# Kernel tuning notes

Hardware: AMD Instinct MI355X
Metric: run time of the kernel (lower is better)

Reference implementation:

```python
import jax, jax.numpy as jnp
import numpy as np

NNZ = 819200
NUM_SESS = 16384
ITEMS_NUM = 1000000
EMB_DIM = 64


def setup_inputs() -> dict:
    key = jax.random.key(0)
    k1, k2, k3, k4 = jax.random.split(key, 4)
    row_idx = jnp.sort(jax.random.randint(k1, (NNZ,), 0, NUM_SESS, dtype=jnp.int32))
    col_idx = jax.random.randint(k2, (NNZ,), 0, ITEMS_NUM, dtype=jnp.int32)
    data_tensor = jax.random.uniform(k3, (NNZ,), dtype=jnp.float32)
    embeddings = jax.random.normal(k4, (ITEMS_NUM, EMB_DIM), dtype=jnp.float32)
    return {
        "row_idx": row_idx,
        "col_idx": col_idx,
        "data_tensor": data_tensor,
        "num_ids": NUM_SESS,
        "embeddings": embeddings,
    }


def reference(row_idx, col_idx, data_tensor, num_ids, embeddings):
    # sparse_coo([num_ids, ITEMS_NUM]) @ embeddings
    # == per-session weighted sum of gathered item embeddings.
    gathered = embeddings[col_idx]                      # [nnz, d]
    weighted = gathered * data_tensor[:, None]          # [nnz, d]
    user_embeddings = jax.ops.segment_sum(
        weighted, row_idx, num_segments=num_ids)        # [num_ids, d]
    return user_embeddings
```

## Files before the change

### kernel.cpp

```cpp
#include <hip/hip_runtime.h>


__global__ __launch_bounds__(256) void build_rowptr_kernel(
    const int* __restrict__ row_idx,
    int*       __restrict__ row_ptr,
    int nnz, int num_sess)
{
    int j = blockIdx.x * blockDim.x + threadIdx.x;
    if (j >= nnz) return;
    int r = row_idx[j];
    if (j == 0) {
        for (int s = 0; s <= r; ++s) row_ptr[s] = 0;
    } else {
        int rp = row_idx[j - 1];
        for (int s = rp + 1; s <= r; ++s) row_ptr[s] = j;
    }
    if (j == nnz - 1) {
        for (int s = r + 1; s <= num_sess; ++s) row_ptr[s] = nnz;
    }
}

__global__ __launch_bounds__(256, 8) void wsum_sess_kernel(
    const int*   __restrict__ row_ptr,
    const int*   __restrict__ col_idx,
    const float* __restrict__ data,
    const float* __restrict__ emb,
    float*       __restrict__ out,
    int num_sess)
{
    const int wave = threadIdx.x >> 6;
    const int lane = threadIdx.x & 63;
    const int sess = (blockIdx.x << 2) + wave;
    if (sess >= num_sess) return;

    const int start = row_ptr[sess];
    const int end   = row_ptr[sess + 1];

    float acc = 0.0f;

    for (int j0 = start; j0 < end; j0 += 64) {
        const int jl    = j0 + lane;
        const bool valid = (jl < end);
        int   col = valid ? col_idx[jl] : 0;
        float w   = valid ? data[jl]    : 0.0f;
        const int rem = end - j0;

        #pragma unroll
        for (int kb = 0; kb < 64; kb += 32) {
            if (kb >= rem) break;
            float v[32];
            float wk[32];
            #pragma unroll
            for (int k = 0; k < 32; ++k) {
                int c = __builtin_amdgcn_readlane(col, kb + k);
                wk[k] = __int_as_float(
                            __builtin_amdgcn_readlane(__float_as_int(w), kb + k));
                v[k] = emb[(size_t)c * 64 + lane];
            }
            #pragma unroll
            for (int k = 0; k < 32; ++k)
                acc += wk[k] * v[k];
        }
    }

    out[(size_t)sess * 64 + lane] = acc;
}

extern "C" void kernel_launch(void* const* d_in, const int* in_sizes, int n_in,
                              void* d_out, int out_size, void* d_ws, size_t ws_size,
                              hipStream_t stream) {
    const int*   row_idx = (const int*)  d_in[0];
    const int*   col_idx = (const int*)  d_in[1];
    const float* data    = (const float*)d_in[2];
    const float* emb     = (const float*)d_in[4];

    const int nnz      = in_sizes[0];
    const int num_sess = out_size / 64;

    int* row_ptr = (int*)d_ws;

    build_rowptr_kernel<<<(nnz + 255) / 256, 256, 0, stream>>>(
        row_idx, row_ptr, nnz, num_sess);

    const int blocks = (num_sess + 3) / 4;
    wsum_sess_kernel<<<blocks, 256, 0, stream>>>(
        row_ptr, col_idx, data, emb, (float*)d_out, num_sess);
}
```

Measured before the change: 335.7 us.

## Bucket nonzeros by embedding row and stream the table through shared memory

Replaces the random per-nonzero embedding gather with a bucket sort of nonzeros by column block. A histogram, a scan and a scatter group the nonzeros by bucket. A materialize kernel then loads each 128-row window of the embedding table into shared memory and writes the weighted rows to a per-nonzero scratch buffer, and a final kernel segment-sums that buffer per session. The aim is to turn scattered row reads into sequential streaming of the table. The cost is reading the entire table, a large scratch write and re-read, extra atomics and several more launches, and it needs a much larger workspace.

Result: slower. 546.2 us (+62.7%).

```diff
diff --git a/kernel.cpp b/kernel.cpp
--- a/kernel.cpp
+++ b/kernel.cpp
@@ -1,12 +1,18 @@
 #include <hip/hip_runtime.h>
+#include <stdint.h>
 
 
-__global__ __launch_bounds__(256) void build_rowptr_kernel(
+#define RPB      128
+#define LOG_RPB  7
+
+__global__ __launch_bounds__(256) void k1_rowptr_hist(
     const int* __restrict__ row_idx,
-    int*       __restrict__ row_ptr,
+    const int* __restrict__ col_idx,
+    int* __restrict__ row_ptr,
+    int* __restrict__ hist,
     int nnz, int num_sess)
 {
-    int j = blockIdx.x * blockDim.x + threadIdx.x;
+    int j = blockIdx.x * 256 + threadIdx.x;
     if (j >= nnz) return;
     int r = row_idx[j];
     if (j == 0) {
@@ -18,52 +24,130 @@
     if (j == nnz - 1) {
         for (int s = r + 1; s <= num_sess; ++s) row_ptr[s] = nnz;
     }
+    atomicAdd(&hist[col_idx[j] >> LOG_RPB], 1);
 }
 
-__global__ __launch_bounds__(256, 8) void wsum_sess_kernel(
-    const int*   __restrict__ row_ptr,
+__global__ __launch_bounds__(1024) void k2_scan(
+    const int* __restrict__ hist,
+    int* __restrict__ bstart,
+    int* __restrict__ cursor,
+    int nb)
+{
+    __shared__ int tsum[1024];
+    int t = threadIdx.x;
+    int loc[8];
+    int base = t * 8;
+    int s = 0;
+    #pragma unroll
+    for (int k = 0; k < 8; ++k) {
+        int b = base + k;
+        int v = (b < nb) ? hist[b] : 0;
+        loc[k] = s;
+        s += v;
+    }
+    tsum[t] = s;
+    __syncthreads();
+    for (int off = 1; off < 1024; off <<= 1) {
+        int v = (t >= off) ? tsum[t - off] : 0;
+        __syncthreads();
+        tsum[t] += v;
+        __syncthreads();
+    }
+    int tbase = (t == 0) ? 0 : tsum[t - 1];
+    #pragma unroll
+    for (int k = 0; k < 8; ++k) {
+        int b = base + k;
+        if (b < nb) {
+            int st = tbase + loc[k];
+            bstart[b] = st;
+            cursor[b] = st;
+        }
+    }
+    if (t == 1023) bstart[nb] = tsum[1023];
+}
+
+__global__ __launch_bounds__(256) void k3_scatter(
     const int*   __restrict__ col_idx,
     const float* __restrict__ data,
-    const float* __restrict__ emb,
+    int*    __restrict__ cursor,
+    float2* __restrict__ colw,
+    int*    __restrict__ jidx,
+    int nnz)
+{
+    int j = blockIdx.x * 256 + threadIdx.x;
+    if (j >= nnz) return;
+    int   c = col_idx[j];
+    float w = data[j];
+    int pos = atomicAdd(&cursor[c >> LOG_RPB], 1);
+    colw[pos] = make_float2(__int_as_float(c), w);
+    jidx[pos] = j;
+}
+
+__global__ __launch_bounds__(256) void k4_materialize(
+    const float4* __restrict__ emb4,
+    const float2* __restrict__ colw,
+    const int*    __restrict__ jidx,
+    const int*    __restrict__ bstart,
+    float*        __restrict__ wscratch,
+    int items)
+{
+    __shared__ float4 win[RPB * 16];
+    const int b = blockIdx.x;
+    const int t = threadIdx.x;
+
+    const size_t gbase = (size_t)b * (RPB * 16);
+    const size_t glim  = (size_t)items * 16;
+    #pragma unroll
+    for (int k = 0; k < 8; ++k) {
+        int li = t + k * 256;
+        size_t gi = gbase + li;
+        if (gi < glim) win[li] = emb4[gi];
+    }
+    __syncthreads();
+
+    const float* winf = (const float*)win;
+    const int bs = bstart[b], be = bstart[b + 1];
+    const int wv = t >> 6, lane = t & 63;
+
+    for (int i = bs + wv; i < be; i += 4) {
+        float2 cw = colw[i];
+        int    c  = __float_as_int(cw.x);
+        int    j  = jidx[i];
+        float  v  = winf[(c & (RPB - 1)) * 64 + lane];
+        wscratch[(size_t)j * 64 + lane] = cw.y * v;
+    }
+}
+
+__global__ __launch_bounds__(256, 8) void k5_segsum(
+    const int*   __restrict__ row_ptr,
+    const float* __restrict__ wscratch,
     float*       __restrict__ out,
     int num_sess)
 {
-    const int wave = threadIdx.x >> 6;
+    const int wv   = threadIdx.x >> 6;
     const int lane = threadIdx.x & 63;
-    const int sess = (blockIdx.x << 2) + wave;
+    const int sess = (blockIdx.x << 2) + wv;
     if (sess >= num_sess) return;
 
-    const int start = row_ptr[sess];
-    const int end   = row_ptr[sess + 1];
+    const int s = row_ptr[sess], e = row_ptr[sess + 1];
+    const int n = e - s;
+    const float* p = wscratch + (size_t)s * 64 + lane;
 
-    float acc = 0.0f;
+    float a0 = 0.f, a1 = 0.f, a2 = 0.f, a3 = 0.f;
+    int k = 0;
+    for (; k + 4 <= n; k += 4) {
+        a0 += p[(size_t)(k + 0) * 64];
+        a1 += p[(size_t)(k + 1) * 64];
+        a2 += p[(size_t)(k + 2) * 64];
+        a3 += p[(size_t)(k + 3) * 64];
+    }
+    for (; k < n; ++k) a0 += p[(size_t)k * 64];
 
-    for (int j0 = start; j0 < end; j0 += 64) {
-        const int jl    = j0 + lane;
-        const bool valid = (jl < end);
-        int   col = valid ? col_idx[jl] : 0;
-        float w   = valid ? data[jl]    : 0.0f;
-        const int rem = end - j0;
+    out[(size_t)sess * 64 + lane] = (a0 + a1) + (a2 + a3);
+}
 
-        #pragma unroll
-        for (int kb = 0; kb < 64; kb += 32) {
-            if (kb >= rem) break;
-            float v[32];
-            float wk[32];
-            #pragma unroll
-            for (int k = 0; k < 32; ++k) {
-                int c = __builtin_amdgcn_readlane(col, kb + k);
-                wk[k] = __int_as_float(
-                            __builtin_amdgcn_readlane(__float_as_int(w), kb + k));
-                v[k] = emb[(size_t)c * 64 + lane];
-            }
-            #pragma unroll
-            for (int k = 0; k < 32; ++k)
-                acc += wk[k] * v[k];
-        }
-    }
-
-    out[(size_t)sess * 64 + lane] = acc;
+static inline char* align256(char* p) {
+    return (char*)(((uintptr_t)p + 255) & ~(uintptr_t)255);
 }
 
 extern "C" void kernel_launch(void* const* d_in, const int* in_sizes, int n_in,
@@ -76,13 +160,38 @@
 
     const int nnz      = in_sizes[0];
     const int num_sess = out_size / 64;
+    const int items    = in_sizes[4] / 64;
+    const int nb       = (items + RPB - 1) >> LOG_RPB;
 
-    int* row_ptr = (int*)d_ws;
+    char* p = (char*)d_ws;
+    float* wscratch = (float*)p;            p += (size_t)nnz * 64 * sizeof(float);
+    p = align256(p);
+    int* row_ptr = (int*)p;                 p += (size_t)(num_sess + 1) * sizeof(int);
+    p = align256(p);
+    int* hist = (int*)p;                    p += (size_t)nb * sizeof(int);
+    p = align256(p);
+    int* bstart = (int*)p;                  p += (size_t)(nb + 1) * sizeof(int);
+    p = align256(p);
+    int* cursor = (int*)p;                  p += (size_t)nb * sizeof(int);
+    p = align256(p);
+    float2* colw = (float2*)p;              p += (size_t)nnz * sizeof(float2);
+    p = align256(p);
+    int* jidx = (int*)p;                    p += (size_t)nnz * sizeof(int);
 
-    build_rowptr_kernel<<<(nnz + 255) / 256, 256, 0, stream>>>(
-        row_idx, row_ptr, nnz, num_sess);
+    hipMemsetAsync(hist, 0, (size_t)nb * sizeof(int), stream);
 
-    const int blocks = (num_sess + 3) / 4;
-    wsum_sess_kernel<<<blocks, 256, 0, stream>>>(
-        row_ptr, col_idx, data, emb, (float*)d_out, num_sess);
+    const int jblocks = (nnz + 255) / 256;
+    k1_rowptr_hist<<<jblocks, 256, 0, stream>>>(
+        row_idx, col_idx, row_ptr, hist, nnz, num_sess);
+
+    k2_scan<<<1, 1024, 0, stream>>>(hist, bstart, cursor, nb);
+
+    k3_scatter<<<jblocks, 256, 0, stream>>>(
+        col_idx, data, cursor, colw, jidx, nnz);
+
+    k4_materialize<<<nb, 256, 0, stream>>>(
+        (const float4*)emb, colw, jidx, bstart, wscratch, items);
+
+    k5_segsum<<<(num_sess + 3) / 4, 256, 0, stream>>>(
+        row_ptr, wscratch, (float*)d_out, num_sess);
 }
```
